# Kernel optimization log

Hardware: AMD Instinct MI355X
Metric: run time of the kernel (lower is better)

The kernel has to match this reference:

```python
import jax, jax.numpy as jnp
import numpy as np

EPS = 1e-5

def setup_inputs() -> dict:
    key = jax.random.key(0)
    ks = jax.random.split(key, 7)
    C = 512
    x = jax.random.normal(ks[0], (16, C, 32, 32), dtype=jnp.float32)
    gn_w = jax.random.normal(ks[1], (C,), dtype=jnp.float32) * 0.02 + 1.0
    gn_b = jax.random.normal(ks[2], (C,), dtype=jnp.float32) * 0.02
    qkv_w = jax.random.normal(ks[3], (3 * C, C), dtype=jnp.float32) * (1.0 / np.sqrt(C))
    qkv_b = jax.random.normal(ks[4], (3 * C,), dtype=jnp.float32) * 0.02
    proj_w = jax.random.normal(ks[5], (C, C), dtype=jnp.float32) * (1.0 / np.sqrt(C))
    proj_b = jax.random.normal(ks[6], (C,), dtype=jnp.float32) * 0.02
    return {"x": x, "gn_w": gn_w, "gn_b": gn_b, "qkv_w": qkv_w,
            "qkv_b": qkv_b, "proj_w": proj_w, "proj_b": proj_b}

def reference(x, gn_w, gn_b, qkv_w, qkv_b, proj_w, proj_b):
    B, C, H, W = x.shape
    S = H * W
    # GroupNorm with 1 group: normalize over (C,H,W) per sample
    mean = jnp.mean(x, axis=(1, 2, 3), keepdims=True)
    var = jnp.var(x, axis=(1, 2, 3), keepdims=True)
    h = (x - mean) * jax.lax.rsqrt(var + EPS)
    h = h * gn_w[None, :, None, None] + gn_b[None, :, None, None]
    # 1x1 conv qkv: [B,C,H,W] -> [B,3C,H,W], flatten spatial -> [B,S,3C]
    hf = h.reshape(B, C, S)  # b c s
    qkv = jnp.einsum('bcs,oc->bso', hf, qkv_w) + qkv_b  # [B,S,3C]
    q, k, v = jnp.split(qkv, 3, axis=-1)  # each [B,S,C]
    scale = C ** (-0.5)
    attn = jax.nn.softmax(jnp.einsum('bqc,bkc->bqk', q, k) * scale, axis=-1)
    out = jnp.einsum('bqk,bkc->bqc', attn, v)  # [B,S,C]
    out = jnp.einsum('bsc,oc->bso', out, proj_w) + proj_b
    out = out.transpose(0, 2, 1).reshape(B, C, H, W)
    return x + out
```

## Files before the change

kernel.cpp:

```cpp
#include <hip/hip_runtime.h>
#include <stdint.h>

#define B_  16
#define C_  512
#define S_  1024
#define NSAMP (C_*S_)

typedef __bf16 bf16x8 __attribute__((ext_vector_type(8)));
typedef float  f32x4  __attribute__((ext_vector_type(4)));

__device__ __forceinline__ float bf2f(uint16_t u){ return __uint_as_float(((uint32_t)u)<<16); }
__device__ __forceinline__ uint16_t f2bf(float f){
  uint32_t u = __float_as_uint(f);
  uint32_t r = u + 0x7fffu + ((u>>16)&1u);
  return (uint16_t)(r>>16);
}
__device__ __forceinline__ float wsum(float v){
  #pragma unroll
  for(int o=32;o;o>>=1) v += __shfl_xor(v,o,64);
  return v;
}
__device__ __forceinline__ int wsumi(int v){
  #pragma unroll
  for(int o=32;o;o>>=1) v += __shfl_xor(v,o,64);
  return v;
}
__device__ __forceinline__ void gload16(const void* g, void* l){
  __builtin_amdgcn_global_load_lds(
      (__attribute__((address_space(1))) void*)g,
      (__attribute__((address_space(3))) void*)l, 16, 0, 0);
}

__device__ __forceinline__ void convseg(const void* src, uint16_t* dst, int n, int f, int t){
  const int idx = t*8;
  if (idx >= n) return;
  if (f){
    const float* s = (const float*)src;
    float4 v0 = *(const float4*)(s + idx);
    float4 v1 = *(const float4*)(s + idx + 4);
    ushort4 a, b;
    a.x=f2bf(v0.x); a.y=f2bf(v0.y); a.z=f2bf(v0.z); a.w=f2bf(v0.w);
    b.x=f2bf(v1.x); b.y=f2bf(v1.y); b.z=f2bf(v1.z); b.w=f2bf(v1.w);
    *(ushort4*)(dst + idx)     = a;
    *(ushort4*)(dst + idx + 4) = b;
  } else {
    *(uint4*)(dst + idx) = *(const uint4*)((const uint16_t*)src + idx);
  }
}
__global__ __launch_bounds__(256) void prep_k(
    const void* __restrict__ srcx, uint16_t* __restrict__ xb, float2* __restrict__ part,
    const void* qkvw, const void* projw, const void* gnw, const void* gnb,
    const void* qkvb, const void* projb,
    uint16_t* qkvwb, uint16_t* projwb, uint16_t* gnwb, uint16_t* gnbb,
    uint16_t* qkvbb, uint16_t* projbb, int* __restrict__ flag){
  const int t = threadIdx.x;
  __shared__ int sdet[4];
  int f;
  {
    const uint4 v = ((const uint4*)srcx)[t & 255];
    uint32_t ww[4] = {v.x, v.y, v.z, v.w};
    int c = 0;
    #pragma unroll
    for(int q=0;q<4;q++) c += ((((ww[q] & 0xffffu) >> 7) & 0xffu) >= 132) ? 1 : 0;
    c = wsumi(c);
    if ((t & 63) == 0) sdet[t >> 6] = c;
    __syncthreads();
    f = (sdet[0] + sdet[1] + sdet[2] + sdet[3] > 128) ? 1 : 0;
  }
  if (blockIdx.x == 0 && t == 0) *flag = f;

  if (blockIdx.x >= 1024){
    const int bid = blockIdx.x - 1024;
    if (bid < 384){
      const size_t off = (size_t)bid*2048;
      convseg((const char*)qkvw + off*(f?4:2), qkvwb + off, 2048, f, t);
    } else if (bid < 512){
      const size_t off = (size_t)(bid-384)*2048;
      convseg((const char*)projw + off*(f?4:2), projwb + off, 2048, f, t);
    } else {
      convseg(gnw,   gnwb,   512,  f, t);
      convseg(gnb,   gnbb,   512,  f, t);
      convseg(qkvb,  qkvbb,  1536, f, t);
      convseg(projb, projbb, 512,  f, t);
    }
    return;
  }
  const size_t base = (size_t)blockIdx.x * 8192;
  float s = 0.f, s2 = 0.f;
  if (f){
    const float4* sp = (const float4*)((const float*)srcx + base);
    ushort4* dp = (ushort4*)(xb + base);
    #pragma unroll
    for(int i=0;i<8;i++){
      float4 v = sp[i*256 + t];
      s  += v.x + v.y + v.z + v.w;
      s2 += v.x*v.x + v.y*v.y + v.z*v.z + v.w*v.w;
      ushort4 o; o.x=f2bf(v.x); o.y=f2bf(v.y); o.z=f2bf(v.z); o.w=f2bf(v.w);
      dp[i*256 + t] = o;
    }
  } else {
    const uint4* sp = (const uint4*)((const uint16_t*)srcx + base);
    uint4* dp = (uint4*)(xb + base);
    #pragma unroll
    for(int i=0;i<4;i++){
      uint4 p = sp[i*256 + t];
      dp[i*256 + t] = p;
      uint32_t uu[4] = {p.x,p.y,p.z,p.w};
      #pragma unroll
      for(int q=0;q<4;q++){
        float f0 = __uint_as_float(uu[q]<<16);
        float f1 = __uint_as_float(uu[q] & 0xffff0000u);
        s += f0 + f1; s2 += f0*f0 + f1*f1;
      }
    }
  }
  s = wsum(s); s2 = wsum(s2);
  __shared__ float rs[4], rq[4];
  const int lane = t & 63, w = t >> 6;
  if (lane==0){ rs[w]=s; rq[w]=s2; }
  __syncthreads();
  if (t==0)
    part[blockIdx.x] = make_float2(rs[0]+rs[1]+rs[2]+rs[3], rq[0]+rq[1]+rq[2]+rq[3]);
}

__global__ __launch_bounds__(256) void gn_apply_t(const uint16_t* __restrict__ x,
    const uint16_t* __restrict__ gw, const uint16_t* __restrict__ gb,
    const float2* __restrict__ part, uint16_t* __restrict__ hT){
  __shared__ float tile[64*129];
  const int b = blockIdx.z, c0 = blockIdx.y<<6, s0 = blockIdx.x<<7;
  const int t = threadIdx.x;
  float2 p = part[b*64 + (t & 63)];
  float s = wsum(p.x), s2 = wsum(p.y);
  const float ninv = 1.f/(float)NSAMP;
  const float mn = s*ninv;
  const float rstd = rsqrtf(s2*ninv - mn*mn + 1e-5f);
  #pragma unroll
  for(int k=0;k<4;k++){
    const int ci = t + k*256;
    const int cl = ci>>4, sc = ci&15;
    uint4 v = *(const uint4*)&x[((size_t)b*C_ + c0+cl)*S_ + s0 + sc*8];
    const uint16_t* e = (const uint16_t*)&v;
    float* dst = &tile[cl*129 + sc*8];
    #pragma unroll
    for(int q=0;q<8;q++) dst[q] = bf2f(e[q]);
  }
  __syncthreads();
  const int cc = t & 7;
  const int sb0 = t >> 3;
  uint4 wv4 = *(const uint4*)&gw[c0 + cc*8];
  uint4 bv4 = *(const uint4*)&gb[c0 + cc*8];
  const uint16_t* we = (const uint16_t*)&wv4;
  const uint16_t* be = (const uint16_t*)&bv4;
  float aq[8], cq[8];
  #pragma unroll
  for(int q=0;q<8;q++){ aq[q] = bf2f(we[q])*rstd; cq[q] = bf2f(be[q]) - mn*aq[q]; }
  #pragma unroll
  for(int k=0;k<4;k++){
    const int sl = sb0 + k*32;
    uint16_t ov[8];
    #pragma unroll
    for(int q=0;q<8;q++){
      float xv = tile[(cc*8+q)*129 + sl];
      ov[q] = f2bf(xv*aq[q] + cq[q]);
    }
    uint4 o;
    o.x = (uint32_t)ov[0] | ((uint32_t)ov[1]<<16);
    o.y = (uint32_t)ov[2] | ((uint32_t)ov[3]<<16);
    o.z = (uint32_t)ov[4] | ((uint32_t)ov[5]<<16);
    o.w = (uint32_t)ov[6] | ((uint32_t)ov[7]<<16);
    *(uint4*)&hT[((size_t)b*S_ + s0+sl)*C_ + c0 + cc*8] = o;
  }
}

__global__ __launch_bounds__(256)
void qkv_k(const uint16_t* __restrict__ hT, const uint16_t* __restrict__ qkvw,
           const uint16_t* __restrict__ qkvb, uint16_t* __restrict__ qk,
           uint16_t* __restrict__ Vt)
{
  __shared__ uint16_t smem[32768];
  const int tid = threadIdx.x;
  const int lane = tid & 63, w = tid >> 6;
  const int quad = lane >> 4, lm = lane & 15;
  const int wm = (w & 1) << 6, wn = (w >> 1) << 6;

  const bool vpath = blockIdx.x >= 1024;
  const int id = vpath ? (blockIdx.x - 1024) : blockIdx.x;
  const int r8 = id & 7, k8 = id >> 3;
  int m0, n0, bz;
  const uint16_t *Abase, *Bbase;
  if (!vpath){
    const int g = r8*16 + (k8 & 15);
    m0 = g << 7; n0 = (k8 >> 4) << 7; bz = 0;
    Abase = hT + (size_t)m0*512;
    Bbase = qkvw + (size_t)n0*512;
  } else {
    const int g = r8*16 + (k8 & 15);
    m0 = (k8 >> 4) << 7; n0 = (g & 7) << 7; bz = g >> 3;
    Abase = qkvw + (size_t)(1024 + m0)*512;
    Bbase = hT + (size_t)bz*S_*C_ + (size_t)n0*512;
  }

  f32x4 acc[4][4];
  #pragma unroll
  for(int i=0;i<4;i++)
    #pragma unroll
    for(int j=0;j<4;j++) acc[i][j] = (f32x4){0.f,0.f,0.f,0.f};

  const int srow = tid >> 3;
  const int sx   = (tid & 7) ^ (srow & 7);
  const uint16_t* ga = Abase + (size_t)srow*512 + sx*8;
  const uint16_t* gb = Bbase + (size_t)srow*512 + sx*8;
  uint16_t* sa0 = &smem[tid*8];
  uint16_t* sb0 = &smem[8192 + tid*8];
  uint16_t* sa1 = &smem[16384 + tid*8];
  uint16_t* sb1 = &smem[24576 + tid*8];

  #pragma unroll
  for(int i=0;i<4;i++){
    gload16(ga + (size_t)(i*32)*512, sa0 + i*2048);
    gload16(gb + (size_t)(i*32)*512, sb0 + i*2048);
  }
  for(int t=0;t<8;t++){
    if (t < 7){
      uint16_t* na = (t&1) ? sa0 : sa1;
      uint16_t* nb = (t&1) ? sb0 : sb1;
      const int k1 = (t+1)<<6;
      #pragma unroll
      for(int i=0;i<4;i++){
        gload16(ga + (size_t)(i*32)*512 + k1, na + i*2048);
        gload16(gb + (size_t)(i*32)*512 + k1, nb + i*2048);
      }
      asm volatile("s_waitcnt vmcnt(8)" ::: "memory");
    } else {
      asm volatile("s_waitcnt vmcnt(0)" ::: "memory");
    }
    __builtin_amdgcn_s_barrier();
    __builtin_amdgcn_sched_barrier(0);
    const int boff = (t&1) << 14;
    #pragma unroll
    for(int kk=0;kk<64;kk+=32){
      bf16x8 av[4], bv[4];
      #pragma unroll
      for(int i=0;i<4;i++){
        const int row = wm + i*16 + lm;
        av[i] = *(const bf16x8*)&smem[boff + row*64 + ((((kk>>3)+quad) ^ (row&7))<<3)];
      }
      #pragma unroll
      for(int j=0;j<4;j++){
        const int row = wn + j*16 + lm;
        bv[j] = *(const bf16x8*)&smem[boff + 8192 + row*64 + ((((kk>>3)+quad) ^ (row&7))<<3)];
      }
      #pragma unroll
      for(int i=0;i<4;i++)
        #pragma unroll
        for(int j=0;j<4;j++)
          acc[i][j] = __builtin_amdgcn_mfma_f32_16x16x32_bf16(av[i], bv[j], acc[i][j], 0,0,0);
    }
    __builtin_amdgcn_s_barrier();
  }

  uint16_t* Cs = smem;
  if (!vpath){
    #pragma unroll
    for(int j=0;j<4;j++){
      const int col_l = wn + j*16 + lm;
      const float bvv = bf2f(qkvb[n0 + col_l]);
      #pragma unroll
      for(int i=0;i<4;i++){
        const int rl0 = wm + i*16 + (quad<<2);
        #pragma unroll
        for(int r=0;r<4;r++)
          Cs[(rl0+r)*128 + col_l] = f2bf(acc[i][j][r] + bvv);
      }
    }
  } else {
    #pragma unroll
    for(int i=0;i<4;i++){
      const int rl0 = wm + i*16 + (quad<<2);
      #pragma unroll
      for(int r=0;r<4;r++){
        const float bvv = bf2f(qkvb[1024 + m0 + rl0 + r]);
        #pragma unroll
        for(int j=0;j<4;j++)
          Cs[(rl0+r)*128 + wn + j*16 + lm] = f2bf(acc[i][j][r] + bvv);
      }
    }
  }
  __syncthreads();
  uint16_t* base = vpath ? (Vt + (size_t)bz*C_*S_) : qk;
  #pragma unroll
  for(int k=0;k<8;k++){
    const int ci = tid + k*256;
    const int rl = ci>>4, ccc = ci&15;
    *(uint4*)&base[(size_t)(m0+rl)*1024 + n0 + ccc*8] = *(const uint4*)&Cs[rl*128 + ccc*8];
  }
}

template<bool HASBIAS, bool BIASROW, bool OUTDYN, bool HASRES, int SWZMODE, bool EXP, int RSMODE>
__global__ __launch_bounds__(256)
void gemm_bt(const uint16_t* __restrict__ A, const uint16_t* __restrict__ Bt,
             void* __restrict__ Cp, const uint16_t* __restrict__ bias,
             const uint16_t* __restrict__ xres, const int* __restrict__ flag,
             float* __restrict__ rs_part,
             int lda, int ldb, int ldc, int K,
             long long sA, long long sB, long long sC)
{
  __shared__ uint16_t smem[32768];
  const int lin = (blockIdx.z * gridDim.y + blockIdx.y) * gridDim.x + blockIdx.x;
  const int r8 = lin & 7, kk8 = lin >> 3;
  int bx, by, bz;
  if (SWZMODE == 0){
    const int G = (gridDim.y * gridDim.z) >> 3;
    const int g = r8 * G + (kk8 % G);
    bx = kk8 / G; by = g % gridDim.y; bz = g / gridDim.y;
  } else {
    const int G = (gridDim.x * gridDim.z) >> 3;
    const int g = r8 * G + (kk8 % G);
    by = kk8 / G; bx = g % gridDim.x; bz = g / gridDim.x;
  }

  const int tid = threadIdx.x;
  const int lane = tid & 63, w = tid >> 6;
  const int quad = lane >> 4, lm = lane & 15;
  const int m0 = by << 7, n0 = bx << 7;
  A  += (size_t)bz * sA;
  Bt += (size_t)bz * sB;

  f32x4 acc[4][4];
  #pragma unroll
  for(int i=0;i<4;i++)
    #pragma unroll
    for(int j=0;j<4;j++) acc[i][j] = (f32x4){0.f,0.f,0.f,0.f};

  const int wm = (w & 1) << 6, wn = (w >> 1) << 6;
  const int srow = tid >> 3;
  const int sx   = (tid & 7) ^ (srow & 7);
  const uint16_t* ga = A  + (size_t)(m0 + srow)*lda + sx*8;
  const uint16_t* gb = Bt + (size_t)(n0 + srow)*ldb + sx*8;
  uint16_t* sa0 = &smem[tid*8];
  uint16_t* sb0 = &smem[8192 + tid*8];
  uint16_t* sa1 = &smem[16384 + tid*8];
  uint16_t* sb1 = &smem[24576 + tid*8];

  const int NT = K >> 6;
  #pragma unroll
  for(int i=0;i<4;i++){
    gload16(ga + (size_t)(i*32)*lda, sa0 + i*2048);
    gload16(gb + (size_t)(i*32)*ldb, sb0 + i*2048);
  }
  for(int t=0;t<NT;t++){
    if (t < NT-1){
      uint16_t* na = (t&1) ? sa0 : sa1;
      uint16_t* nb = (t&1) ? sb0 : sb1;
      const int k1 = (t+1)<<6;
      #pragma unroll
      for(int i=0;i<4;i++){
        gload16(ga + (size_t)(i*32)*lda + k1, na + i*2048);
        gload16(gb + (size_t)(i*32)*ldb + k1, nb + i*2048);
      }
      asm volatile("s_waitcnt vmcnt(8)" ::: "memory");
    } else {
      asm volatile("s_waitcnt vmcnt(0)" ::: "memory");
    }
    __builtin_amdgcn_s_barrier();
    __builtin_amdgcn_sched_barrier(0);
    const int boff = (t&1) << 14;
    #pragma unroll
    for(int kk=0;kk<64;kk+=32){
      bf16x8 av[4], bv[4];
      #pragma unroll
      for(int i=0;i<4;i++){
        const int row = wm + i*16 + lm;
        av[i] = *(const bf16x8*)&smem[boff + row*64 + ((((kk>>3)+quad) ^ (row&7))<<3)];
      }
      #pragma unroll
      for(int j=0;j<4;j++){
        const int row = wn + j*16 + lm;
        bv[j] = *(const bf16x8*)&smem[boff + 8192 + row*64 + ((((kk>>3)+quad) ^ (row&7))<<3)];
      }
      #pragma unroll
      for(int i=0;i<4;i++)
        #pragma unroll
        for(int j=0;j<4;j++)
          acc[i][j] = __builtin_amdgcn_mfma_f32_16x16x32_bf16(av[i], bv[j], acc[i][j], 0,0,0);
    }
    __builtin_amdgcn_s_barrier();
  }

  const size_t cb = (size_t)bz * (size_t)sC;
  if (!OUTDYN && !HASRES){
    uint16_t* Cs = smem;
    float rp[4][4];
    if (RSMODE == 1){
      #pragma unroll
      for(int i=0;i<4;i++)
        #pragma unroll
        for(int r=0;r<4;r++) rp[i][r] = 0.f;
    }
    float inv[4][4];
    if (RSMODE == 2){
      const int myrow = m0 + wm + lm*4 + quad;
      const float4* rpp = (const float4*)&rs_part[((size_t)bz*1024 + myrow)*16];
      float4 a0 = rpp[0], a1 = rpp[1], a2 = rpp[2], a3 = rpp[3];
      float rowsumv = a0.x+a0.y+a0.z+a0.w + a1.x+a1.y+a1.z+a1.w
                    + a2.x+a2.y+a2.z+a2.w + a3.x+a3.y+a3.z+a3.w;
      #pragma unroll
      for(int i=0;i<4;i++)
        #pragma unroll
        for(int r=0;r<4;r++)
          inv[i][r] = 1.f / __shfl(rowsumv, r*16 + i*4 + quad, 64);
    }
    #pragma unroll
    for(int j=0;j<4;j++){
      const int col_l = wn + j*16 + lm;
      const float cbias = (HASBIAS && !BIASROW) ? bf2f(bias[n0 + col_l]) : 0.f;
      #pragma unroll
      for(int i=0;i<4;i++){
        const int rl0 = wm + i*16 + (quad<<2);
        #pragma unroll
        for(int r=0;r<4;r++){
          float v = acc[i][j][r] + cbias;
          if (HASBIAS && BIASROW) v += bf2f(bias[m0 + rl0 + r]);
          if (EXP)          v = __expf(v * 0.044194173824159216f);
          if (RSMODE == 1)  rp[i][r] += v;
          if (RSMODE == 2)  v *= inv[i][r];
          Cs[(rl0+r)*128 + col_l] = f2bf(v);
        }
      }
    }
    if (RSMODE == 1){
      #pragma unroll
      for(int i=0;i<4;i++)
        #pragma unroll
        for(int r=0;r<4;r++){
          float s4 = rp[i][r];
          #pragma unroll
          for(int o=8;o;o>>=1) s4 += __shfl_xor(s4, o, 64);
          if (lm == 0)
            rs_part[((size_t)bz*1024 + m0 + wm + i*16 + (quad<<2) + r)*16 + (bx<<1) + (w>>1)] = s4;
        }
    }
    __syncthreads();
    uint16_t* base = (uint16_t*)Cp + cb;
    #pragma unroll
    for(int k=0;k<8;k++){
      const int ci = tid + k*256;
      const int rl = ci>>4, cc = ci&15;
      *(uint4*)&base[(size_t)(m0+rl)*ldc + n0 + cc*8] = *(const uint4*)&Cs[rl*128 + cc*8];
    }
  } else {
    float* Cs32 = (float*)smem;
    const int f = OUTDYN ? *flag : 0;
    const int wnh = wn >> 1;
    #pragma unroll
    for(int half=0; half<2; ++half){
      #pragma unroll
      for(int j2=0;j2<2;j2++){
        const int j = half*2 + j2;
        const int col_l = wn + j*16 + lm;
        const int hcol = wnh + j2*16 + lm;
        const float cbias = (HASBIAS && !BIASROW) ? bf2f(bias[n0 + col_l]) : 0.f;
        #pragma unroll
        for(int i=0;i<4;i++){
          const int rl0 = wm + i*16 + (quad<<2);
          #pragma unroll
          for(int r=0;r<4;r++){
            float v = acc[i][j][r] + cbias;
            if (HASBIAS && BIASROW) v += bf2f(bias[m0 + rl0 + r]);
            if (EXP) v = __expf(v * 0.044194173824159216f);
            Cs32[(rl0+r)*64 + hcol] = v;
          }
        }
      }
      __syncthreads();
      #pragma unroll
      for(int k=0;k<8;k++){
        const int ci = tid + k*256;
        const int rl = ci>>4, c4 = ci&15;
        float4 vv = *(const float4*)&Cs32[rl*64 + c4*4];
        const int gcol = n0 + c4*4 + ((c4>=8)?32:0) + half*32;
        const size_t idx = cb + (size_t)(m0+rl)*ldc + gcol;
        float o0=vv.x, o1=vv.y, o2=vv.z, o3=vv.w;
        if (HASRES){
          uint2 rr = *(const uint2*)&xres[idx];
          o0 += bf2f((uint16_t)(rr.x & 0xffffu));
          o1 += bf2f((uint16_t)(rr.x >> 16));
          o2 += bf2f((uint16_t)(rr.y & 0xffffu));
          o3 += bf2f((uint16_t)(rr.y >> 16));
        }
        if (OUTDYN && f){
          float4 o = make_float4(o0,o1,o2,o3);
          *(float4*)&((float*)Cp)[idx] = o;
        } else {
          uint2 o;
          o.x = (uint32_t)f2bf(o0) | ((uint32_t)f2bf(o1)<<16);
          o.y = (uint32_t)f2bf(o2) | ((uint32_t)f2bf(o3)<<16);
          *(uint2*)&((uint16_t*)Cp)[idx] = o;
        }
      }
      __syncthreads();
    }
  }
}

extern "C" void kernel_launch(void* const* d_in, const int* in_sizes, int n_in,
                              void* d_out, int out_size, void* d_ws, size_t ws_size,
                              hipStream_t stream){
  char* ws = (char*)d_ws;
  int*      flag  = (int*)ws;
  float2*   part  = (float2*)(ws + 4096);
  uint16_t* gnwb  = (uint16_t*)(ws + 16384);
  uint16_t* gnbb  = (uint16_t*)(ws + 17408);
  uint16_t* qkvbb = (uint16_t*)(ws + 18432);
  uint16_t* projbb= (uint16_t*)(ws + 21504);
  uint16_t* qkvwb = (uint16_t*)(ws + 32768);
  uint16_t* projwb= (uint16_t*)(ws + 1605632);
  float*    rs_part=(float*)  (ws + 2129920);
  uint16_t* xb    = (uint16_t*)(ws + 4194304);
  uint16_t* hT    = (uint16_t*)(ws + 20971520);
  uint16_t* qk    = (uint16_t*)(ws + 37748736);
  uint16_t* sc    = (uint16_t*)(ws + 71303168);
  uint16_t* Vt    = (uint16_t*)(ws + 104857600);

  hipLaunchKernelGGL(prep_k, dim3(1537), dim3(256), 0, stream,
                     d_in[0], xb, part,
                     d_in[3], d_in[5], d_in[1], d_in[2], d_in[4], d_in[6],
                     qkvwb, projwb, gnwb, gnbb, qkvbb, projbb, flag);
  hipLaunchKernelGGL(gn_apply_t, dim3(8,8,16), dim3(256), 0, stream, xb, gnwb, gnbb, part, hT);

  hipLaunchKernelGGL(qkv_k, dim3(1536), dim3(256), 0, stream, hT, qkvwb, qkvbb, qk, Vt);

  hipLaunchKernelGGL((gemm_bt<false,false,false,false,0,true,1>), dim3(8,8,16), dim3(256), 0, stream,
      qk, qk + 512, (void*)sc, (const uint16_t*)nullptr, (const uint16_t*)nullptr, flag, rs_part,
      1024, 1024, 1024, 512, (long long)S_*1024, (long long)S_*1024, (long long)S_*S_);

  hipLaunchKernelGGL((gemm_bt<false,false,false,false,0,false,2>), dim3(4,8,16), dim3(256), 0, stream,
      sc, Vt, (void*)hT, (const uint16_t*)nullptr, (const uint16_t*)nullptr, flag, rs_part,
      1024, 1024, 512, 1024, (long long)S_*S_, (long long)C_*S_, (long long)S_*C_);

  hipLaunchKernelGGL((gemm_bt<true,true,true,true,1,false,0>), dim3(8,4,16), dim3(256), 0, stream,
      projwb, hT, d_out, projbb, xb, flag, (float*)nullptr,
      512, 512, 1024, 512, 0LL, (long long)S_*C_, (long long)C_*S_);
}
```

Before: 204.3 us.

## Fuse QK^T, softmax and PV into a single flash-attention style kernel

```diff
diff --git a/kernel.cpp b/kernel.cpp
--- a/kernel.cpp
+++ b/kernel.cpp
@@ -296,12 +296,211 @@
   }
 }
 
-template<bool HASBIAS, bool BIASROW, bool OUTDYN, bool HASRES, int SWZMODE, bool EXP, int RSMODE>
+__global__ __launch_bounds__(512)
+void fa_k(const uint16_t* __restrict__ qk, const uint16_t* __restrict__ Vt,
+          uint16_t* __restrict__ out)
+{
+  extern __shared__ char smem[];
+  uint16_t* Qs = (uint16_t*)smem;
+  char* Pb = smem + 65536;
+  char* ST = smem + 81920;
+  float* RS = (float*)(smem + 147456);
+
+  const int tid = threadIdx.x;
+  const int w = tid >> 6, lane = tid & 63;
+  const int quad = lane >> 4, lm = lane & 15;
+  const int wq = w & 1, wk = w >> 1;
+
+  const int wg = (blockIdx.x & 7)*32 + (blockIdx.x >> 3);
+  const int bz = wg >> 4;
+  const int q0 = (wg & 15) << 6;
+
+  const uint16_t* qbase = qk + ((size_t)bz*1024 + q0)*1024;
+  const uint16_t* kbase = qk + (size_t)bz*1024*1024 + 512;
+  const uint16_t* vbase = Vt + ((size_t)bz*512 + w*64)*1024;
+
+  f32x4 o[4][4];
+  #pragma unroll
+  for(int i=0;i<4;i++)
+    #pragma unroll
+    for(int j=0;j<4;j++) o[i][j] = (f32x4){0.f,0.f,0.f,0.f};
+  float rsacc[2][4];
+  #pragma unroll
+  for(int i=0;i<2;i++)
+    #pragma unroll
+    for(int r=0;r<4;r++) rsacc[i][r] = 0.f;
+
+  auto stage_k = [&](int kt, int ch){
+    #pragma unroll
+    for (int g=0; g<2; ++g){
+      const int idx = g*512 + tid;
+      const int row = idx >> 3, c8 = idx & 7;
+      gload16(kbase + (size_t)(kt*128 + row)*1024 + ch*64 + ((c8 ^ (row&7))<<3),
+              ST + ((ch&3)<<14) + idx*16);
+    }
+  };
+  auto stage_v = [&](int kt, int kk){
+    #pragma unroll
+    for (int g=0; g<4; ++g){
+      const int idx = g*64 + lane;
+      const int c = idx >> 2, c4 = idx & 3;
+      gload16(vbase + (size_t)c*1024 + kt*128 + kk*32 + ((c4 ^ (c&3))<<3),
+              ST + ((kk&1)<<15) + (w<<12) + idx*16);
+    }
+  };
+
+  #pragma unroll
+  for (int rd=0; rd<8; ++rd){
+    const int row = rd*8 + (tid>>6), chunk = tid & 63;
+    const int scol = (chunk & 56) | ((chunk & 7) ^ (row & 7));
+    gload16(qbase + (size_t)row*1024 + scol*8, (char*)Qs + rd*8192 + tid*16);
+  }
+  stage_k(0,0); stage_k(0,1); stage_k(0,2);
+
+  for (int kt=0; kt<8; ++kt){
+    f32x4 s[2][2];
+    #pragma unroll
+    for(int i=0;i<2;i++)
+      #pragma unroll
+      for(int j=0;j<2;j++) s[i][j] = (f32x4){0.f,0.f,0.f,0.f};
+
+    #pragma unroll
+    for (int ch=0; ch<8; ++ch){
+      if (ch==6) asm volatile("s_waitcnt vmcnt(2)" ::: "memory");
+      else       asm volatile("s_waitcnt vmcnt(4)" ::: "memory");
+      __builtin_amdgcn_s_barrier();
+      __builtin_amdgcn_sched_barrier(0);
+      if (ch < 5) stage_k(kt, ch+3);
+      if (ch == 6) stage_v(kt, 0);
+      const int slot = (ch&3)<<14;
+      #pragma unroll
+      for (int kk=0; kk<2; ++kk){
+        bf16x8 av[2], bv[2];
+        #pragma unroll
+        for (int i=0;i<2;i++){
+          const int q = wq*32 + i*16 + lm;
+          av[i] = *(const bf16x8*)((const char*)Qs + q*1024 + (ch*8 + (((kk<<2)+quad) ^ (q&7)))*16);
+        }
+        #pragma unroll
+        for (int j=0;j<2;j++){
+          const int key = wk*32 + j*16 + lm;
+          bv[j] = *(const bf16x8*)(ST + slot + key*128 + ((((kk<<2)+quad) ^ (key&7))<<4));
+        }
+        #pragma unroll
+        for (int i=0;i<2;i++)
+          #pragma unroll
+          for (int j=0;j<2;j++)
+            s[i][j] = __builtin_amdgcn_mfma_f32_16x16x32_bf16(av[i], bv[j], s[i][j], 0,0,0);
+      }
+    }
+
+    #pragma unroll
+    for (int i=0;i<2;i++)
+      #pragma unroll
+      for (int j=0;j<2;j++)
+        #pragma unroll
+        for (int r=0;r<4;r++){
+          const int q = wq*32 + i*16 + (quad<<2) + r;
+          const int col = wk*32 + j*16 + lm;
+          const float pv = __expf(s[i][j][r] * 0.044194173824159216f);
+          rsacc[i][r] += pv;
+          const int cch = col >> 3;
+          const int chs = (cch & 8) | ((cch & 7) ^ (q & 7));
+          *(uint16_t*)(Pb + q*256 + chs*16 + ((col & 7)<<1)) = f2bf(pv);
+        }
+    asm volatile("s_waitcnt lgkmcnt(0)" ::: "memory");
+    __builtin_amdgcn_sched_barrier(0);
+    __builtin_amdgcn_s_barrier();
+    __builtin_amdgcn_sched_barrier(0);
+    stage_v(kt, 1);
+
+    #pragma unroll
+    for (int kk=0; kk<4; ++kk){
+      if (kk<3) asm volatile("s_waitcnt vmcnt(4)" ::: "memory");
+      else      asm volatile("s_waitcnt vmcnt(0)" ::: "memory");
+      __builtin_amdgcn_sched_barrier(0);
+      bf16x8 pa[4], bv[4];
+      #pragma unroll
+      for (int i=0;i<4;i++){
+        const int q = i*16 + lm;
+        const int cch = (kk<<2) + quad;
+        const int chs = (cch & 8) | ((cch & 7) ^ (q & 7));
+        pa[i] = *(const bf16x8*)(Pb + q*256 + chs*16);
+      }
+      #pragma unroll
+      for (int j=0;j<4;j++){
+        const int c = j*16 + lm;
+        bv[j] = *(const bf16x8*)(ST + ((kk&1)<<15) + (w<<12) + c*64 + ((quad ^ (c&3))<<4));
+      }
+      #pragma unroll
+      for (int i=0;i<4;i++)
+        #pragma unroll
+        for (int j=0;j<4;j++)
+          o[i][j] = __builtin_amdgcn_mfma_f32_16x16x32_bf16(pa[i], bv[j], o[i][j], 0,0,0);
+      __builtin_amdgcn_sched_barrier(0);
+      if (kk<2) stage_v(kt, kk+2);
+    }
+    __builtin_amdgcn_s_barrier();
+    if (kt < 7){ stage_k(kt+1,0); stage_k(kt+1,1); stage_k(kt+1,2); }
+  }
+
+  #pragma unroll
+  for (int i=0;i<2;i++)
+    #pragma unroll
+    for (int r=0;r<4;r++){
+      float v = rsacc[i][r];
+      #pragma unroll
+      for (int off=1; off<16; off<<=1) v += __shfl_xor(v, off, 64);
+      rsacc[i][r] = v;
+    }
+  if (lm == 0){
+    #pragma unroll
+    for (int i=0;i<2;i++)
+      #pragma unroll
+      for (int r=0;r<4;r++){
+        const int q = wq*32 + i*16 + (quad<<2) + r;
+        RS[q*4 + wk] = rsacc[i][r];
+      }
+  }
+  asm volatile("s_waitcnt lgkmcnt(0)" ::: "memory");
+  __builtin_amdgcn_sched_barrier(0);
+  __builtin_amdgcn_s_barrier();
+  __builtin_amdgcn_sched_barrier(0);
+  float inv_[4][4];
+  #pragma unroll
+  for (int i=0;i<4;i++)
+    #pragma unroll
+    for (int r=0;r<4;r++){
+      const int q = i*16 + (quad<<2) + r;
+      f32x4 rv = *(const f32x4*)&RS[q*4];
+      inv_[i][r] = 1.f / (rv[0]+rv[1]+rv[2]+rv[3]);
+    }
+  uint16_t* Cs = Qs;
+  #pragma unroll
+  for (int i=0;i<4;i++)
+    #pragma unroll
+    for (int j=0;j<4;j++)
+      #pragma unroll
+      for (int r=0;r<4;r++){
+        const int row = i*16 + (quad<<2) + r;
+        const int col = (w<<6) + j*16 + lm;
+        Cs[row*512 + col] = f2bf(o[i][j][r] * inv_[i][r]);
+      }
+  __syncthreads();
+  #pragma unroll
+  for (int rd=0; rd<8; ++rd){
+    const int idx = rd*512 + tid;
+    const int row = idx >> 6, cc = idx & 63;
+    *(uint4*)&out[((size_t)bz*1024 + q0 + row)*512 + cc*8] =
+        *(const uint4*)((const char*)Cs + row*1024 + cc*16);
+  }
+}
+
+template<bool HASBIAS, bool BIASROW, bool OUTDYN, bool HASRES, int SWZMODE, bool EXP>
 __global__ __launch_bounds__(256)
 void gemm_bt(const uint16_t* __restrict__ A, const uint16_t* __restrict__ Bt,
              void* __restrict__ Cp, const uint16_t* __restrict__ bias,
              const uint16_t* __restrict__ xres, const int* __restrict__ flag,
-             float* __restrict__ rs_part,
              int lda, int ldb, int ldc, int K,
              long long sA, long long sB, long long sC)
 {
@@ -390,26 +589,6 @@
   const size_t cb = (size_t)bz * (size_t)sC;
   if (!OUTDYN && !HASRES){
     uint16_t* Cs = smem;
-    float rp[4][4];
-    if (RSMODE == 1){
-      #pragma unroll
-      for(int i=0;i<4;i++)
-        #pragma unroll
-        for(int r=0;r<4;r++) rp[i][r] = 0.f;
-    }
-    float inv[4][4];
-    if (RSMODE == 2){
-      const int myrow = m0 + wm + lm*4 + quad;
-      const float4* rpp = (const float4*)&rs_part[((size_t)bz*1024 + myrow)*16];
-      float4 a0 = rpp[0], a1 = rpp[1], a2 = rpp[2], a3 = rpp[3];
-      float rowsumv = a0.x+a0.y+a0.z+a0.w + a1.x+a1.y+a1.z+a1.w
-                    + a2.x+a2.y+a2.z+a2.w + a3.x+a3.y+a3.z+a3.w;
-      #pragma unroll
-      for(int i=0;i<4;i++)
-        #pragma unroll
-        for(int r=0;r<4;r++)
-          inv[i][r] = 1.f / __shfl(rowsumv, r*16 + i*4 + quad, 64);
-    }
     #pragma unroll
     for(int j=0;j<4;j++){
       const int col_l = wn + j*16 + lm;
@@ -421,24 +600,10 @@
         for(int r=0;r<4;r++){
           float v = acc[i][j][r] + cbias;
           if (HASBIAS && BIASROW) v += bf2f(bias[m0 + rl0 + r]);
-          if (EXP)          v = __expf(v * 0.044194173824159216f);
-          if (RSMODE == 1)  rp[i][r] += v;
-          if (RSMODE == 2)  v *= inv[i][r];
+          if (EXP) v = __expf(v * 0.044194173824159216f);
           Cs[(rl0+r)*128 + col_l] = f2bf(v);
         }
       }
-    }
-    if (RSMODE == 1){
-      #pragma unroll
-      for(int i=0;i<4;i++)
-        #pragma unroll
-        for(int r=0;r<4;r++){
-          float s4 = rp[i][r];
-          #pragma unroll
-          for(int o=8;o;o>>=1) s4 += __shfl_xor(s4, o, 64);
-          if (lm == 0)
-            rs_part[((size_t)bz*1024 + m0 + wm + i*16 + (quad<<2) + r)*16 + (bx<<1) + (w>>1)] = s4;
-        }
     }
     __syncthreads();
     uint16_t* base = (uint16_t*)Cp + cb;
@@ -489,13 +654,13 @@
           o3 += bf2f((uint16_t)(rr.y >> 16));
         }
         if (OUTDYN && f){
-          float4 o = make_float4(o0,o1,o2,o3);
-          *(float4*)&((float*)Cp)[idx] = o;
+          float4 oo = make_float4(o0,o1,o2,o3);
+          *(float4*)&((float*)Cp)[idx] = oo;
         } else {
-          uint2 o;
-          o.x = (uint32_t)f2bf(o0) | ((uint32_t)f2bf(o1)<<16);
-          o.y = (uint32_t)f2bf(o2) | ((uint32_t)f2bf(o3)<<16);
-          *(uint2*)&((uint16_t*)Cp)[idx] = o;
+          uint2 oo;
+          oo.x = (uint32_t)f2bf(o0) | ((uint32_t)f2bf(o1)<<16);
+          oo.y = (uint32_t)f2bf(o2) | ((uint32_t)f2bf(o3)<<16);
+          *(uint2*)&((uint16_t*)Cp)[idx] = oo;
         }
       }
       __syncthreads();
@@ -515,12 +680,17 @@
   uint16_t* projbb= (uint16_t*)(ws + 21504);
   uint16_t* qkvwb = (uint16_t*)(ws + 32768);
   uint16_t* projwb= (uint16_t*)(ws + 1605632);
-  float*    rs_part=(float*)  (ws + 2129920);
   uint16_t* xb    = (uint16_t*)(ws + 4194304);
   uint16_t* hT    = (uint16_t*)(ws + 20971520);
   uint16_t* qk    = (uint16_t*)(ws + 37748736);
-  uint16_t* sc    = (uint16_t*)(ws + 71303168);
   uint16_t* Vt    = (uint16_t*)(ws + 104857600);
+
+  static bool attr_done = false;
+  if (!attr_done){
+    (void)hipFuncSetAttribute(reinterpret_cast<const void*>(fa_k),
+                              hipFuncAttributeMaxDynamicSharedMemorySize, 148480);
+    attr_done = true;
+  }
 
   hipLaunchKernelGGL(prep_k, dim3(1537), dim3(256), 0, stream,
                      d_in[0], xb, part,
@@ -530,15 +700,9 @@
 
   hipLaunchKernelGGL(qkv_k, dim3(1536), dim3(256), 0, stream, hT, qkvwb, qkvbb, qk, Vt);
 
-  hipLaunchKernelGGL((gemm_bt<false,false,false,false,0,true,1>), dim3(8,8,16), dim3(256), 0, stream,
-      qk, qk + 512, (void*)sc, (const uint16_t*)nullptr, (const uint16_t*)nullptr, flag, rs_part,
-      1024, 1024, 1024, 512, (long long)S_*1024, (long long)S_*1024, (long long)S_*S_);
-
-  hipLaunchKernelGGL((gemm_bt<false,false,false,false,0,false,2>), dim3(4,8,16), dim3(256), 0, stream,
-      sc, Vt, (void*)hT, (const uint16_t*)nullptr, (const uint16_t*)nullptr, flag, rs_part,
-      1024, 1024, 512, 1024, (long long)S_*S_, (long long)C_*S_, (long long)S_*C_);
-
-  hipLaunchKernelGGL((gemm_bt<true,true,true,true,1,false,0>), dim3(8,4,16), dim3(256), 0, stream,
-      projwb, hT, d_out, projbb, xb, flag, (float*)nullptr,
+  hipLaunchKernelGGL(fa_k, dim3(256), dim3(512), 148480, stream, qk, Vt, hT);
+
+  hipLaunchKernelGGL((gemm_bt<true,true,true,true,1,false>), dim3(8,4,16), dim3(256), 0, stream,
+      projwb, hT, d_out, projbb, xb, flag,
       512, 512, 1024, 512, 0LL, (long long)S_*C_, (long long)C_*S_);
 }
```

Measured after the change: 205.2 us. No clear change (+0.4%).
